# Optimization experiments

Hardware: AMD Instinct MI355X
Metric: run time of the kernel (lower is better)

## Reference

```python
import jax, jax.numpy as jnp
import numpy as np

NUM_HEADS = 16
INPUT_SIZE = 1024
KEY_SIZE = 64
VALUE_SIZE = 64
LN_EPS = 1e-5


def setup_inputs() -> dict:
    key = jax.random.key(0)
    ks = jax.random.split(key, 11)
    B, S, D = 2, 2048, INPUT_SIZE
    Hk = NUM_HEADS * KEY_SIZE
    Hv = NUM_HEADS * VALUE_SIZE
    s = 0.02
    return {
        "queries": jax.random.normal(ks[0], (B, S, D), dtype=jnp.float32),
        "Wq": jax.random.normal(ks[1], (D, Hk), dtype=jnp.float32) * s,
        "bq": jnp.zeros((Hk,), dtype=jnp.float32),
        "Wk": jax.random.normal(ks[2], (D, Hk), dtype=jnp.float32) * s,
        "bk": jnp.zeros((Hk,), dtype=jnp.float32),
        "Wv": jax.random.normal(ks[3], (D, Hv), dtype=jnp.float32) * s,
        "bv": jnp.zeros((Hv,), dtype=jnp.float32),
        "Wo": jax.random.normal(ks[4], (Hv, D), dtype=jnp.float32) * s,
        "bo": jnp.zeros((D,), dtype=jnp.float32),
        "ln_gamma": jnp.ones((D,), dtype=jnp.float32),
        "ln_beta": jnp.zeros((D,), dtype=jnp.float32),
    }


def reference(queries, Wq, bq, Wk, bk, Wv, bv, Wo, bo, ln_gamma, ln_beta):
    B, S, D = queries.shape
    H, dk, dv = NUM_HEADS, KEY_SIZE, VALUE_SIZE
    residual = queries
    # projections -> [B, S, H, d]
    q = (queries @ Wq + bq).reshape(B, S, H, dk)
    k = (queries @ Wk + bk).reshape(B, S, H, dk)
    v = (queries @ Wv + bv).reshape(B, S, H, dv)
    # scaled dot-product attention per head
    scores = jnp.einsum("bqhd,bkhd->bhqk", q, k) / jnp.sqrt(jnp.float32(dk))
    attn = jax.nn.softmax(scores, axis=-1)
    out = jnp.einsum("bhqk,bkhd->bqhd", attn, v).reshape(B, S, H * dv)
    # out projection + residual + layernorm (dropout=0 / eval)
    res = out @ Wo + bo + residual
    mu = jnp.mean(res, axis=-1, keepdims=True)
    var = jnp.var(res, axis=-1, keepdims=True)
    return (res - mu) / jnp.sqrt(var + LN_EPS) * ln_gamma + ln_beta
```

## Files before the change

kernel.cpp:

```cpp
#include <hip/hip_runtime.h>
#include <hip/hip_bf16.h>
#include <math.h>

#define D 1024
#define NH 16
#define DK 64
#define LN_EPS 1e-5f
typedef __hip_bfloat16 bf16;
typedef __attribute__((ext_vector_type(8))) short bf16x8;
typedef __attribute__((ext_vector_type(4))) short short4v;
typedef __attribute__((ext_vector_type(4))) float f32x4;

__device__ inline float tofloat(bf16 x) { return __bfloat162float(x); }
__device__ inline short bfbits(float v) {
    bf16 b = __float2bfloat16(v);
    return __builtin_bit_cast(short, b);
}

template <typename T> __device__ inline T fromfloat(float v);
template <> __device__ inline float fromfloat<float>(float v) { return v; }
template <> __device__ inline bf16 fromfloat<bf16>(float v) { return __float2bfloat16(v); }

__global__ void detect_kernel(const unsigned short* __restrict__ X, int* __restrict__ flag) {
    __shared__ int cnt;
    if (threadIdx.x == 0) cnt = 0;
    __syncthreads();
    int local = 0;
    for (int i = threadIdx.x; i < 4096; i += 256) {
        unsigned short u = X[i];
        if (((u >> 7) & 0xFF) >= 0x90) local++;
    }
    atomicAdd(&cnt, local);
    __syncthreads();
    if (threadIdx.x == 0) flag[0] = (cnt > 8) ? 1 : 0;
}

__global__ void convert_kernel(const void* __restrict__ src, bf16* __restrict__ dst,
                               int n, const int* __restrict__ flag) {
    const int isf32 = flag[0];
    for (int i = blockIdx.x * blockDim.x + threadIdx.x; i < n; i += gridDim.x * blockDim.x) {
        if (isf32) dst[i] = __float2bfloat16(((const float*)src)[i]);
        else       dst[i] = ((const bf16*)src)[i];
    }
}

__global__ void convert_small(const void* s0, const void* s1, const void* s2, const void* s3,
                              const void* s4, const void* s5, bf16* __restrict__ bqkv,
                              bf16* __restrict__ bo, bf16* __restrict__ g, bf16* __restrict__ be,
                              const int* __restrict__ flag) {
    const int isf32 = flag[0];
    int idx = blockIdx.x * 256 + threadIdx.x;
    int seg = idx >> 10, off = idx & 1023;
    const void* srcs[6] = {s0, s1, s2, s3, s4, s5};
    const void* src = srcs[seg];
    float v = isf32 ? ((const float*)src)[off] : tofloat(((const bf16*)src)[off]);
    bf16 bv = __float2bfloat16(v);
    if (seg < 3)      bqkv[seg * 1024 + off] = bv;
    else if (seg == 3) bo[off] = bv;
    else if (seg == 4) g[off] = bv;
    else               be[off] = bv;
}

__global__ void convert_transpose4(const void* s0, const void* s1, const void* s2, const void* s3,
                                   bf16* __restrict__ Wqkvt, bf16* __restrict__ Wot,
                                   const int* __restrict__ flag) {
    __shared__ float tile[64][65];
    const int isf32 = flag[0];
    const int z = blockIdx.z;
    const void* srcs[4] = {s0, s1, s2, s3};
    const void* src = srcs[z];
    bf16* dst = (z < 3) ? (Wqkvt + (size_t)z * 1024 * 1024) : Wot;
    const int i0 = blockIdx.y * 64, j0 = blockIdx.x * 64;
    const int r = threadIdx.x >> 2, c0 = (threadIdx.x & 3) * 16;
#pragma unroll
    for (int i = 0; i < 16; ++i) {
        int c = c0 + i;
        size_t idx = (size_t)(i0 + r) * 1024 + j0 + c;
        tile[r][c] = isf32 ? ((const float*)src)[idx] : tofloat(((const bf16*)src)[idx]);
    }
    __syncthreads();
#pragma unroll
    for (int i = 0; i < 16; ++i) {
        int c = c0 + i;
        dst[(size_t)(j0 + r) * 1024 + i0 + c] = __float2bfloat16(tile[c][r]);
    }
}

template <typename TC, bool RES, bool QS, bool VT>
__global__ __launch_bounds__(256) void mfma_gemm2(const bf16* __restrict__ A, const bf16* __restrict__ Bt,
                                                  const bf16* __restrict__ bias,
                                                  const bf16* __restrict__ residual,
                                                  TC* __restrict__ C, bf16* __restrict__ VtG,
                                                  int M, int N, int K, int S) {
    __shared__ short As[128][72];
    __shared__ short Bs[128][72];
    const int tid = threadIdx.x;
    const int lane = tid & 63, wave = tid >> 6;
    const int wy = wave >> 1, wx = wave & 1;
    const int mrow = lane & 15, quad = lane >> 4;
    const int bm = blockIdx.y * 128, bn = blockIdx.x * 128;

    f32x4 acc[4][4];
#pragma unroll
    for (int mi = 0; mi < 4; ++mi)
#pragma unroll
        for (int nt = 0; nt < 4; ++nt) acc[mi][nt] = (f32x4){0.f, 0.f, 0.f, 0.f};

    const int ra = tid >> 1, ca = (tid & 1) * 32;
    const bf16* aptr = A + (size_t)(bm + ra) * K + ca;
    const bf16* bptr = Bt + (size_t)(bn + ra) * K + ca;
    bf16x8 ar[4], br[4];
#pragma unroll
    for (int i = 0; i < 4; ++i) { ar[i] = *(const bf16x8*)(aptr + i * 8); br[i] = *(const bf16x8*)(bptr + i * 8); }

    for (int k0 = 0; k0 < K; k0 += 64) {
        __syncthreads();
#pragma unroll
        for (int i = 0; i < 4; ++i) {
            *(bf16x8*)&As[ra][ca + i * 8] = ar[i];
            *(bf16x8*)&Bs[ra][ca + i * 8] = br[i];
        }
        __syncthreads();
        if (k0 + 64 < K) {
#pragma unroll
            for (int i = 0; i < 4; ++i) {
                ar[i] = *(const bf16x8*)(aptr + k0 + 64 + i * 8);
                br[i] = *(const bf16x8*)(bptr + k0 + 64 + i * 8);
            }
        }
#pragma unroll
        for (int ks = 0; ks < 2; ++ks) {
            bf16x8 a[4], b[4];
#pragma unroll
            for (int mi = 0; mi < 4; ++mi)
                a[mi] = *(const bf16x8*)&As[wy * 64 + mi * 16 + mrow][ks * 32 + quad * 8];
#pragma unroll
            for (int nt = 0; nt < 4; ++nt)
                b[nt] = *(const bf16x8*)&Bs[wx * 64 + nt * 16 + mrow][ks * 32 + quad * 8];
#pragma unroll
            for (int mi = 0; mi < 4; ++mi)
#pragma unroll
                for (int nt = 0; nt < 4; ++nt)
                    acc[mi][nt] = __builtin_amdgcn_mfma_f32_16x16x32_bf16(a[mi], b[nt], acc[mi][nt], 0, 0, 0);
        }
    }
#pragma unroll
    for (int mi = 0; mi < 4; ++mi) {
#pragma unroll
        for (int nt = 0; nt < 4; ++nt) {
            int col = bn + wx * 64 + nt * 16 + mrow;
            float bc = tofloat(bias[col]);
            if (VT && col >= 2048) {
                int dvf = col - 2048, hh = dvf >> 6, dv = dvf & 63;
                int row0 = bm + wy * 64 + mi * 16 + quad * 4;
                int bb = row0 / S, key = row0 % S;
                short4v pk;
#pragma unroll
                for (int reg = 0; reg < 4; ++reg) pk[reg] = bfbits(acc[mi][nt][reg] + bc);
                *(short4v*)(VtG + ((size_t)(bb * NH + hh) * 64 + dv) * S + key) = pk;
            } else {
                float sc = (QS && col < 1024) ? 0.18033688f : 1.0f;
#pragma unroll
                for (int reg = 0; reg < 4; ++reg) {
                    int row = bm + wy * 64 + mi * 16 + quad * 4 + reg;
                    float v = (acc[mi][nt][reg] + bc) * sc;
                    if (RES) v += tofloat(residual[(size_t)row * N + col]);
                    C[(size_t)row * N + col] = fromfloat<TC>(v);
                }
            }
        }
    }
}

__global__ __launch_bounds__(256) void attn_mfma(const bf16* __restrict__ QKV,
                                                 const bf16* __restrict__ VtG,
                                                 bf16* __restrict__ O, int S) {
    __shared__ short Ks[64][72];
    __shared__ short Vs[64][72];
    const int tid = threadIdx.x;
    const int lane = tid & 63, wave = tid >> 6;
    const int mrow = lane & 15, quad = lane >> 4;
    const int ldq = 3 * D;
    const int nqc = S / 128;
    const int bh = blockIdx.x / nqc, qc = blockIdx.x % nqc;
    const int b = bh / NH, h = bh % NH;
    const int q0 = qc * 128 + wave * 32;

    bf16x8 qf[2][2];
#pragma unroll
    for (int qt = 0; qt < 2; ++qt) {
        const bf16* qbase = QKV + ((size_t)(b * S + q0 + qt * 16 + mrow)) * ldq + h * DK;
        qf[qt][0] = *(const bf16x8*)(qbase + quad * 8);
        qf[qt][1] = *(const bf16x8*)(qbase + 32 + quad * 8);
    }

    f32x4 o[2][4];
#pragma unroll
    for (int qt = 0; qt < 2; ++qt)
#pragma unroll
        for (int t = 0; t < 4; ++t) o[qt][t] = (f32x4){0.f, 0.f, 0.f, 0.f};
    float lsum[2] = {0.f, 0.f};

    const int rs_ = tid >> 2, cs_ = (tid & 3) * 16;
    const bf16* kb0 = QKV + ((size_t)(b * S + rs_)) * ldq + D + h * DK + cs_;
    const bf16* vb0 = VtG + ((size_t)(b * NH + h) * 64 + rs_) * S + cs_;
    bf16x8 kr0 = *(const bf16x8*)kb0, kr1 = *(const bf16x8*)(kb0 + 8);
    bf16x8 vr0 = *(const bf16x8*)vb0, vr1 = *(const bf16x8*)(vb0 + 8);

    for (int kc = 0; kc < S; kc += 64) {
        __syncthreads();
        *(bf16x8*)&Ks[rs_][cs_] = kr0;
        *(bf16x8*)&Ks[rs_][cs_ + 8] = kr1;
        *(bf16x8*)&Vs[rs_][cs_] = vr0;
        *(bf16x8*)&Vs[rs_][cs_ + 8] = vr1;
        __syncthreads();
        if (kc + 64 < S) {
            const bf16* kn = kb0 + (size_t)(kc + 64) * ldq;
            kr0 = *(const bf16x8*)kn; kr1 = *(const bf16x8*)(kn + 8);
            const bf16* vn = vb0 + kc + 64;
            vr0 = *(const bf16x8*)vn; vr1 = *(const bf16x8*)(vn + 8);
        }

        f32x4 s[2][4];
#pragma unroll
        for (int qt = 0; qt < 2; ++qt)
#pragma unroll
            for (int t = 0; t < 4; ++t) s[qt][t] = (f32x4){0.f, 0.f, 0.f, 0.f};
#pragma unroll
        for (int ks = 0; ks < 2; ++ks) {
#pragma unroll
            for (int t = 0; t < 4; ++t) {
                bf16x8 kf = *(const bf16x8*)&Ks[t * 16 + mrow][ks * 32 + quad * 8];
                s[0][t] = __builtin_amdgcn_mfma_f32_16x16x32_bf16(kf, qf[0][ks], s[0][t], 0, 0, 0);
                s[1][t] = __builtin_amdgcn_mfma_f32_16x16x32_bf16(kf, qf[1][ks], s[1][t], 0, 0, 0);
            }
        }
        short4v pf[2][4];
#pragma unroll
        for (int qt = 0; qt < 2; ++qt)
#pragma unroll
            for (int t = 0; t < 4; ++t) {
                float p0 = __builtin_amdgcn_exp2f(s[qt][t][0]);
                float p1 = __builtin_amdgcn_exp2f(s[qt][t][1]);
                float p2 = __builtin_amdgcn_exp2f(s[qt][t][2]);
                float p3 = __builtin_amdgcn_exp2f(s[qt][t][3]);
                lsum[qt] += (p0 + p1) + (p2 + p3);
                short4v pk; pk[0] = bfbits(p0); pk[1] = bfbits(p1); pk[2] = bfbits(p2); pk[3] = bfbits(p3);
                pf[qt][t] = pk;
            }
#pragma unroll
        for (int kt = 0; kt < 4; ++kt) {
#pragma unroll
            for (int dvt = 0; dvt < 4; ++dvt) {
                short4v vf = *(const short4v*)&Vs[dvt * 16 + mrow][kt * 16 + quad * 4];
                o[0][dvt] = __builtin_amdgcn_mfma_f32_16x16x16bf16_1k(pf[0][kt], vf, o[0][dvt], 0, 0, 0);
                o[1][dvt] = __builtin_amdgcn_mfma_f32_16x16x16bf16_1k(pf[1][kt], vf, o[1][dvt], 0, 0, 0);
            }
        }
    }
#pragma unroll
    for (int qt = 0; qt < 2; ++qt) {
        float v = lsum[qt];
        v += __shfl_xor(v, 16, 64);
        v += __shfl_xor(v, 32, 64);
        lsum[qt] = v;
    }
#pragma unroll
    for (int qt = 0; qt < 2; ++qt)
#pragma unroll
        for (int r = 0; r < 4; ++r) {
            float inv = 1.0f / __shfl(lsum[qt], quad * 4 + r, 64);
            bf16* orow = O + ((size_t)(b * S + q0 + qt * 16 + quad * 4 + r)) * D + h * DK;
#pragma unroll
            for (int dvt = 0; dvt < 4; ++dvt)
                orow[dvt * 16 + mrow] = __float2bfloat16(o[qt][dvt][r] * inv);
        }
}

__global__ void ln_kernel(const float* __restrict__ R, const bf16* __restrict__ gamma,
                          const bf16* __restrict__ beta, void* __restrict__ out,
                          const int* __restrict__ flag) {
    __shared__ float red[8];
    const int isf32 = flag[0];
    const int row = blockIdx.x;
    const float4 xv = *(const float4*)(R + (size_t)row * D + threadIdx.x * 4);
    float sum = xv.x + xv.y + xv.z + xv.w;
    float sq = xv.x * xv.x + xv.y * xv.y + xv.z * xv.z + xv.w * xv.w;
    for (int off = 32; off; off >>= 1) {
        sum += __shfl_xor(sum, off, 64);
        sq += __shfl_xor(sq, off, 64);
    }
    const int wave = threadIdx.x / 64, lane = threadIdx.x % 64;
    if (lane == 0) { red[wave] = sum; red[wave + 4] = sq; }
    __syncthreads();
    sum = red[0] + red[1] + red[2] + red[3];
    sq = red[4] + red[5] + red[6] + red[7];
    const float mu = sum / (float)D;
    const float var = sq / (float)D - mu * mu;
    const float inv = rsqrtf(var + LN_EPS);
    const float x4[4] = {xv.x, xv.y, xv.z, xv.w};
#pragma unroll
    for (int i = 0; i < 4; ++i) {
        int cidx = threadIdx.x * 4 + i;
        float y = (x4[i] - mu) * inv * tofloat(gamma[cidx]) + tofloat(beta[cidx]);
        size_t oidx = (size_t)row * D + cidx;
        if (isf32) ((float*)out)[oidx] = y;
        else       ((bf16*)out)[oidx] = __float2bfloat16(y);
    }
}

extern "C" void kernel_launch(void* const* d_in, const int* in_sizes, int n_in,
                              void* d_out, int out_size, void* d_ws, size_t ws_size,
                              hipStream_t stream) {
    const int M = in_sizes[0] / D;
    const int B = 2;
    const int S = M / B;

    char* p = (char*)d_ws;
    auto alloc = [&](size_t bytes) { char* r = p; p += (bytes + 255) & ~(size_t)255; return r; };
    int*  flag  = (int*)alloc(4);
    bf16* Xb    = (bf16*)alloc((size_t)M * D * 2);
    bf16* Wqkvt = (bf16*)alloc((size_t)3 * D * D * 2);
    bf16* Wot   = (bf16*)alloc((size_t)D * D * 2);
    bf16* bqkv  = (bf16*)alloc(3 * D * 2);
    bf16* bob   = (bf16*)alloc(D * 2);
    bf16* gb    = (bf16*)alloc(D * 2);
    bf16* beb   = (bf16*)alloc(D * 2);
    bf16* QKV   = (bf16*)alloc((size_t)M * 3 * D * 2);
    bf16* VtG   = (bf16*)alloc((size_t)M * D * 2);
    bf16* Ob    = (bf16*)alloc((size_t)M * D * 2);
    float* Rf   = (float*)alloc((size_t)M * D * 4);

    detect_kernel<<<1, 256, 0, stream>>>((const unsigned short*)d_in[0], flag);

    convert_kernel<<<4096, 256, 0, stream>>>(d_in[0], Xb, in_sizes[0], flag);
    convert_transpose4<<<dim3(16, 16, 4), 256, 0, stream>>>(d_in[1], d_in[3], d_in[5], d_in[7],
                                                            Wqkvt, Wot, flag);
    convert_small<<<24, 256, 0, stream>>>(d_in[2], d_in[4], d_in[6], d_in[8], d_in[9], d_in[10],
                                          bqkv, bob, gb, beb, flag);

    mfma_gemm2<bf16, false, true, true><<<dim3(3 * D / 128, M / 128), 256, 0, stream>>>(
        Xb, Wqkvt, bqkv, nullptr, QKV, VtG, M, 3 * D, D, S);

    attn_mfma<<<B * NH * (S / 128), 256, 0, stream>>>(QKV, VtG, Ob, S);

    mfma_gemm2<float, true, false, false><<<dim3(D / 128, M / 128), 256, 0, stream>>>(
        Ob, Wot, bob, Xb, Rf, nullptr, M, D, D, S);

    ln_kernel<<<M, 256, 0, stream>>>(Rf, gb, beb, d_out, flag);
}
```

Before: 236.6 us.

## Split attention KV range in two with combine pass, fuse prep kernels

Attention now splits the key/value range into two halves along a second grid dimension. Each half writes unnormalized partial outputs and row sums, and a new combine kernel adds them and normalizes. This doubles the number of attention blocks to improve occupancy, at the cost of extra global traffic for the partial buffers. V is stored in a key-grouped layout with a swizzled shared-memory placement to cut bank conflicts. Detection, input conversion, weight transpose and bias conversion are merged into one prep kernel, and each kernel now detects the input dtype per wave instead of reading a flag, which removes several launches.

Measured after the change: 234.7 us. Within noise of the previous version (-0.8%).

```diff
diff --git a/kernel.cpp b/kernel.cpp
--- a/kernel.cpp
+++ b/kernel.cpp
@@ -10,79 +10,97 @@
 typedef __attribute__((ext_vector_type(8))) short bf16x8;
 typedef __attribute__((ext_vector_type(4))) short short4v;
 typedef __attribute__((ext_vector_type(4))) float f32x4;
+typedef __attribute__((ext_vector_type(2))) unsigned int uint2v;
 
 __device__ inline float tofloat(bf16 x) { return __bfloat162float(x); }
+__device__ inline float tofs(short s) {
+    bf16 b; __builtin_memcpy(&b, &s, 2);
+    return __bfloat162float(b);
+}
 __device__ inline short bfbits(float v) {
     bf16 b = __float2bfloat16(v);
-    return __builtin_bit_cast(short, b);
+    short s; __builtin_memcpy(&s, &b, 2);
+    return s;
+}
+__device__ inline unsigned int pk2(float a, float b) {
+    float2 f2; f2.x = a; f2.y = b;
+    __hip_bfloat162 h = __float22bfloat162_rn(f2);
+    unsigned int u; __builtin_memcpy(&u, &h, 4);
+    return u;
+}
+__device__ inline short4v pk4(float a, float b, float c, float d) {
+    uint2v u; u[0] = pk2(a, b); u[1] = pk2(c, d);
+    short4v s; __builtin_memcpy(&s, &u, 8);
+    return s;
+}
+
+__device__ inline int wave_isf32(const unsigned short* __restrict__ Xu) {
+    unsigned short u = Xu[threadIdx.x & 63];
+    unsigned long long m = __ballot(((u >> 7) & 0xFF) >= 0x90);
+    return __popcll(m) > 2;
 }
 
 template <typename T> __device__ inline T fromfloat(float v);
 template <> __device__ inline float fromfloat<float>(float v) { return v; }
 template <> __device__ inline bf16 fromfloat<bf16>(float v) { return __float2bfloat16(v); }
 
-__global__ void detect_kernel(const unsigned short* __restrict__ X, int* __restrict__ flag) {
-    __shared__ int cnt;
-    if (threadIdx.x == 0) cnt = 0;
-    __syncthreads();
-    int local = 0;
-    for (int i = threadIdx.x; i < 4096; i += 256) {
-        unsigned short u = X[i];
-        if (((u >> 7) & 0xFF) >= 0x90) local++;
-    }
-    atomicAdd(&cnt, local);
-    __syncthreads();
-    if (threadIdx.x == 0) flag[0] = (cnt > 8) ? 1 : 0;
-}
-
-__global__ void convert_kernel(const void* __restrict__ src, bf16* __restrict__ dst,
-                               int n, const int* __restrict__ flag) {
-    const int isf32 = flag[0];
-    for (int i = blockIdx.x * blockDim.x + threadIdx.x; i < n; i += gridDim.x * blockDim.x) {
-        if (isf32) dst[i] = __float2bfloat16(((const float*)src)[i]);
-        else       dst[i] = ((const bf16*)src)[i];
-    }
-}
-
-__global__ void convert_small(const void* s0, const void* s1, const void* s2, const void* s3,
-                              const void* s4, const void* s5, bf16* __restrict__ bqkv,
-                              bf16* __restrict__ bo, bf16* __restrict__ g, bf16* __restrict__ be,
-                              const int* __restrict__ flag) {
-    const int isf32 = flag[0];
-    int idx = blockIdx.x * 256 + threadIdx.x;
-    int seg = idx >> 10, off = idx & 1023;
-    const void* srcs[6] = {s0, s1, s2, s3, s4, s5};
-    const void* src = srcs[seg];
-    float v = isf32 ? ((const float*)src)[off] : tofloat(((const bf16*)src)[off]);
-    bf16 bv = __float2bfloat16(v);
-    if (seg < 3)      bqkv[seg * 1024 + off] = bv;
-    else if (seg == 3) bo[off] = bv;
-    else if (seg == 4) g[off] = bv;
-    else               be[off] = bv;
-}
-
-__global__ void convert_transpose4(const void* s0, const void* s1, const void* s2, const void* s3,
-                                   bf16* __restrict__ Wqkvt, bf16* __restrict__ Wot,
-                                   const int* __restrict__ flag) {
+__global__ void prep_kernel(const void* X, const void* Wq, const void* Wk, const void* Wv,
+                            const void* Wo, const void* bq, const void* bk, const void* bv,
+                            const void* bo, const void* g, const void* be,
+                            bf16* __restrict__ Xb, bf16* __restrict__ Wqkvt, bf16* __restrict__ Wot,
+                            bf16* __restrict__ bqkv, bf16* __restrict__ bob,
+                            bf16* __restrict__ gb, bf16* __restrict__ beb) {
     __shared__ float tile[64][65];
-    const int isf32 = flag[0];
-    const int z = blockIdx.z;
-    const void* srcs[4] = {s0, s1, s2, s3};
-    const void* src = srcs[z];
-    bf16* dst = (z < 3) ? (Wqkvt + (size_t)z * 1024 * 1024) : Wot;
-    const int i0 = blockIdx.y * 64, j0 = blockIdx.x * 64;
-    const int r = threadIdx.x >> 2, c0 = (threadIdx.x & 3) * 16;
-#pragma unroll
-    for (int i = 0; i < 16; ++i) {
-        int c = c0 + i;
-        size_t idx = (size_t)(i0 + r) * 1024 + j0 + c;
-        tile[r][c] = isf32 ? ((const float*)src)[idx] : tofloat(((const bf16*)src)[idx]);
-    }
-    __syncthreads();
-#pragma unroll
-    for (int i = 0; i < 16; ++i) {
-        int c = c0 + i;
-        dst[(size_t)(j0 + r) * 1024 + i0 + c] = __float2bfloat16(tile[c][r]);
+    const int isf32 = wave_isf32((const unsigned short*)X);
+    const int bid = blockIdx.x;
+    if (bid < 2048) {
+        int e0 = bid * 2048 + threadIdx.x * 8;
+        bf16x8 outv;
+        if (isf32) {
+            float4 v0 = ((const float4*)X)[e0 / 4];
+            float4 v1 = ((const float4*)X)[e0 / 4 + 1];
+            uint2v a, b;
+            a[0] = pk2(v0.x, v0.y); a[1] = pk2(v0.z, v0.w);
+            b[0] = pk2(v1.x, v1.y); b[1] = pk2(v1.z, v1.w);
+            short4v s0, s1;
+            __builtin_memcpy(&s0, &a, 8); __builtin_memcpy(&s1, &b, 8);
+#pragma unroll
+            for (int i = 0; i < 4; ++i) { outv[i] = s0[i]; outv[4 + i] = s1[i]; }
+        } else {
+            outv = ((const bf16x8*)X)[e0 / 8];
+        }
+        *(bf16x8*)(Xb + e0) = outv;
+    } else if (bid < 3072) {
+        int t = bid - 2048;
+        int z = t >> 8, rem = t & 255;
+        const void* srcs[4] = {Wq, Wk, Wv, Wo};
+        const void* src = srcs[z];
+        bf16* dst = (z < 3) ? (Wqkvt + (size_t)z * 1024 * 1024) : Wot;
+        const int i0 = (rem >> 4) * 64, j0 = (rem & 15) * 64;
+        const int r = threadIdx.x >> 2, c0 = (threadIdx.x & 3) * 16;
+#pragma unroll
+        for (int i = 0; i < 16; ++i) {
+            int c = c0 + i;
+            size_t idx = (size_t)(i0 + r) * 1024 + j0 + c;
+            tile[r][c] = isf32 ? ((const float*)src)[idx] : tofloat(((const bf16*)src)[idx]);
+        }
+        __syncthreads();
+#pragma unroll
+        for (int i = 0; i < 16; ++i) {
+            int c = c0 + i;
+            dst[(size_t)(j0 + r) * 1024 + i0 + c] = __float2bfloat16(tile[c][r]);
+        }
+    } else {
+        int idx = (bid - 3072) * 256 + threadIdx.x;
+        int seg = idx >> 10, off = idx & 1023;
+        const void* srcs[6] = {bq, bk, bv, bo, g, be};
+        const void* src = srcs[seg];
+        float v = isf32 ? ((const float*)src)[off] : tofloat(((const bf16*)src)[off]);
+        bf16 bv16 = __float2bfloat16(v);
+        if (seg < 3)       bqkv[seg * 1024 + off] = bv16;
+        else if (seg == 3) bob[off] = bv16;
+        else if (seg == 4) gb[off] = bv16;
+        else               beb[off] = bv16;
     }
 }
 
@@ -153,11 +171,10 @@
             if (VT && col >= 2048) {
                 int dvf = col - 2048, hh = dvf >> 6, dv = dvf & 63;
                 int row0 = bm + wy * 64 + mi * 16 + quad * 4;
-                int bb = row0 / S, key = row0 % S;
-                short4v pk;
-#pragma unroll
-                for (int reg = 0; reg < 4; ++reg) pk[reg] = bfbits(acc[mi][nt][reg] + bc);
-                *(short4v*)(VtG + ((size_t)(bb * NH + hh) * 64 + dv) * S + key) = pk;
+                int bb = row0 / S, key0 = row0 % S;
+                short4v pk = pk4(acc[mi][nt][0] + bc, acc[mi][nt][1] + bc,
+                                 acc[mi][nt][2] + bc, acc[mi][nt][3] + bc);
+                *(short4v*)(VtG + (size_t)(bb * NH + hh) * S * 64 + (key0 >> 2) * 256 + dv * 4) = pk;
             } else {
                 float sc = (QS && col < 1024) ? 0.18033688f : 1.0f;
 #pragma unroll
@@ -174,9 +191,10 @@
 
 __global__ __launch_bounds__(256) void attn_mfma(const bf16* __restrict__ QKV,
                                                  const bf16* __restrict__ VtG,
-                                                 bf16* __restrict__ O, int S) {
+                                                 bf16* __restrict__ Op, float* __restrict__ Lp,
+                                                 int S, int M) {
     __shared__ short Ks[64][72];
-    __shared__ short Vs[64][72];
+    __shared__ short Vs2[16 * 256];
     const int tid = threadIdx.x;
     const int lane = tid & 63, wave = tid >> 6;
     const int mrow = lane & 15, quad = lane >> 4;
@@ -185,6 +203,8 @@
     const int bh = blockIdx.x / nqc, qc = blockIdx.x % nqc;
     const int b = bh / NH, h = bh % NH;
     const int q0 = qc * 128 + wave * 32;
+    const int sp = blockIdx.y;
+    const int Sh = S / 2, kvlo = sp * Sh;
 
     bf16x8 qf[2][2];
 #pragma unroll
@@ -202,22 +222,24 @@
     float lsum[2] = {0.f, 0.f};
 
     const int rs_ = tid >> 2, cs_ = (tid & 3) * 16;
-    const bf16* kb0 = QKV + ((size_t)(b * S + rs_)) * ldq + D + h * DK + cs_;
-    const bf16* vb0 = VtG + ((size_t)(b * NH + h) * 64 + rs_) * S + cs_;
+    const bf16* kb0 = QKV + ((size_t)(b * S + kvlo + rs_)) * ldq + D + h * DK + cs_;
+    const bf16* vb0 = VtG + (size_t)(b * NH + h) * S * 64 + kvlo * 64 + tid * 16;
+    const int kg_l = tid >> 4, dv0 = (tid & 15) * 4;
+    const int voff = kg_l * 256 + (((dv0 + kg_l * 8) & 63) * 4);
     bf16x8 kr0 = *(const bf16x8*)kb0, kr1 = *(const bf16x8*)(kb0 + 8);
     bf16x8 vr0 = *(const bf16x8*)vb0, vr1 = *(const bf16x8*)(vb0 + 8);
 
-    for (int kc = 0; kc < S; kc += 64) {
+    for (int kc = 0; kc < Sh; kc += 64) {
         __syncthreads();
         *(bf16x8*)&Ks[rs_][cs_] = kr0;
         *(bf16x8*)&Ks[rs_][cs_ + 8] = kr1;
-        *(bf16x8*)&Vs[rs_][cs_] = vr0;
-        *(bf16x8*)&Vs[rs_][cs_ + 8] = vr1;
-        __syncthreads();
-        if (kc + 64 < S) {
+        *(bf16x8*)&Vs2[voff] = vr0;
+        *(bf16x8*)&Vs2[voff + 8] = vr1;
+        __syncthreads();
+        if (kc + 64 < Sh) {
             const bf16* kn = kb0 + (size_t)(kc + 64) * ldq;
             kr0 = *(const bf16x8*)kn; kr1 = *(const bf16x8*)(kn + 8);
-            const bf16* vn = vb0 + kc + 64;
+            const bf16* vn = vb0 + (size_t)(kc + 64) * 64;
             vr0 = *(const bf16x8*)vn; vr1 = *(const bf16x8*)(vn + 8);
         }
 
@@ -245,14 +267,15 @@
                 float p2 = __builtin_amdgcn_exp2f(s[qt][t][2]);
                 float p3 = __builtin_amdgcn_exp2f(s[qt][t][3]);
                 lsum[qt] += (p0 + p1) + (p2 + p3);
-                short4v pk; pk[0] = bfbits(p0); pk[1] = bfbits(p1); pk[2] = bfbits(p2); pk[3] = bfbits(p3);
-                pf[qt][t] = pk;
+                pf[qt][t] = pk4(p0, p1, p2, p3);
             }
 #pragma unroll
         for (int kt = 0; kt < 4; ++kt) {
+            const int kg = kt * 4 + quad;
 #pragma unroll
             for (int dvt = 0; dvt < 4; ++dvt) {
-                short4v vf = *(const short4v*)&Vs[dvt * 16 + mrow][kt * 16 + quad * 4];
+                int dvs = ((dvt * 16 + mrow) + kg * 8) & 63;
+                short4v vf = *(const short4v*)&Vs2[kg * 256 + dvs * 4];
                 o[0][dvt] = __builtin_amdgcn_mfma_f32_16x16x16bf16_1k(pf[0][kt], vf, o[0][dvt], 0, 0, 0);
                 o[1][dvt] = __builtin_amdgcn_mfma_f32_16x16x16bf16_1k(pf[1][kt], vf, o[1][dvt], 0, 0, 0);
             }
@@ -264,24 +287,43 @@
         v += __shfl_xor(v, 16, 64);
         v += __shfl_xor(v, 32, 64);
         lsum[qt] = v;
+        if (quad == 0) Lp[(size_t)sp * M + b * S + q0 + qt * 16 + mrow] = v;
     }
 #pragma unroll
     for (int qt = 0; qt < 2; ++qt)
 #pragma unroll
         for (int r = 0; r < 4; ++r) {
-            float inv = 1.0f / __shfl(lsum[qt], quad * 4 + r, 64);
-            bf16* orow = O + ((size_t)(b * S + q0 + qt * 16 + quad * 4 + r)) * D + h * DK;
+            bf16* orow = Op + (size_t)sp * M * D +
+                         ((size_t)(b * S + q0 + qt * 16 + quad * 4 + r)) * D + h * DK;
 #pragma unroll
             for (int dvt = 0; dvt < 4; ++dvt)
-                orow[dvt * 16 + mrow] = __float2bfloat16(o[qt][dvt][r] * inv);
-        }
+                orow[dvt * 16 + mrow] = __float2bfloat16(o[qt][dvt][r]);
+        }
+}
+
+__global__ void combine_kernel(const bf16* __restrict__ Op, const float* __restrict__ Lp,
+                               bf16* __restrict__ Ob, int M) {
+    int idx = blockIdx.x * 256 + threadIdx.x;
+    int row = idx >> 7;
+    size_t e0 = (size_t)row * D + (idx & 127) * 8;
+    bf16x8 o0 = *(const bf16x8*)(Op + e0);
+    bf16x8 o1 = *(const bf16x8*)(Op + (size_t)M * D + e0);
+    float inv = 1.0f / (Lp[row] + Lp[M + row]);
+    float f[8];
+#pragma unroll
+    for (int i = 0; i < 8; ++i) f[i] = (tofs(o0[i]) + tofs(o1[i])) * inv;
+    bf16x8 outv;
+    short4v a = pk4(f[0], f[1], f[2], f[3]), b2 = pk4(f[4], f[5], f[6], f[7]);
+#pragma unroll
+    for (int i = 0; i < 4; ++i) { outv[i] = a[i]; outv[4 + i] = b2[i]; }
+    *(bf16x8*)(Ob + e0) = outv;
 }
 
 __global__ void ln_kernel(const float* __restrict__ R, const bf16* __restrict__ gamma,
                           const bf16* __restrict__ beta, void* __restrict__ out,
-                          const int* __restrict__ flag) {
+                          const void* __restrict__ X) {
     __shared__ float red[8];
-    const int isf32 = flag[0];
+    const int isf32 = wave_isf32((const unsigned short*)X);
     const int row = blockIdx.x;
     const float4 xv = *(const float4*)(R + (size_t)row * D + threadIdx.x * 4);
     float sum = xv.x + xv.y + xv.z + xv.w;
@@ -318,7 +360,6 @@
 
     char* p = (char*)d_ws;
     auto alloc = [&](size_t bytes) { char* r = p; p += (bytes + 255) & ~(size_t)255; return r; };
-    int*  flag  = (int*)alloc(4);
     bf16* Xb    = (bf16*)alloc((size_t)M * D * 2);
     bf16* Wqkvt = (bf16*)alloc((size_t)3 * D * D * 2);
     bf16* Wot   = (bf16*)alloc((size_t)D * D * 2);
@@ -328,24 +369,24 @@
     bf16* beb   = (bf16*)alloc(D * 2);
     bf16* QKV   = (bf16*)alloc((size_t)M * 3 * D * 2);
     bf16* VtG   = (bf16*)alloc((size_t)M * D * 2);
+    bf16* Opart = (bf16*)alloc((size_t)2 * M * D * 2);
+    float* Lp   = (float*)alloc((size_t)2 * M * 4);
     bf16* Ob    = (bf16*)alloc((size_t)M * D * 2);
     float* Rf   = (float*)alloc((size_t)M * D * 4);
 
-    detect_kernel<<<1, 256, 0, stream>>>((const unsigned short*)d_in[0], flag);
-
-    convert_kernel<<<4096, 256, 0, stream>>>(d_in[0], Xb, in_sizes[0], flag);
-    convert_transpose4<<<dim3(16, 16, 4), 256, 0, stream>>>(d_in[1], d_in[3], d_in[5], d_in[7],
-                                                            Wqkvt, Wot, flag);
-    convert_small<<<24, 256, 0, stream>>>(d_in[2], d_in[4], d_in[6], d_in[8], d_in[9], d_in[10],
-                                          bqkv, bob, gb, beb, flag);
+    prep_kernel<<<3096, 256, 0, stream>>>(d_in[0], d_in[1], d_in[3], d_in[5], d_in[7],
+                                          d_in[2], d_in[4], d_in[6], d_in[8], d_in[9], d_in[10],
+                                          Xb, Wqkvt, Wot, bqkv, bob, gb, beb);
 
     mfma_gemm2<bf16, false, true, true><<<dim3(3 * D / 128, M / 128), 256, 0, stream>>>(
         Xb, Wqkvt, bqkv, nullptr, QKV, VtG, M, 3 * D, D, S);
 
-    attn_mfma<<<B * NH * (S / 128), 256, 0, stream>>>(QKV, VtG, Ob, S);
+    attn_mfma<<<dim3(B * NH * (S / 128), 2), 256, 0, stream>>>(QKV, VtG, Opart, Lp, S, M);
+
+    combine_kernel<<<M * D / 8 / 256, 256, 0, stream>>>(Opart, Lp, Ob, M);
 
     mfma_gemm2<float, true, false, false><<<dim3(D / 128, M / 128), 256, 0, stream>>>(
         Ob, Wot, bob, Xb, Rf, nullptr, M, D, D, S);
 
-    ln_kernel<<<M, 256, 0, stream>>>(Rf, gb, beb, d_out, flag);
-}
+    ln_kernel<<<M, 256, 0, stream>>>(Rf, gb, beb, d_out, d_in[0]);
+}
```
